# Kernel tuning notes

Hardware: AMD Instinct MI355X
Metric: run time of the kernel (lower is better)

The kernel has to match this reference:

```python
import jax, jax.numpy as jnp
import numpy as np

HEADS = 16
HEAD_DIM = 128


def rotate_half(x):
    x1, x2 = jnp.split(x, 2, axis=-1)
    return jnp.concatenate((-x2, x1), axis=-1)


def setup_inputs() -> dict:
    key = jax.random.key(0)
    ks = jax.random.split(key, 8)
    b, s, h = 2, 2048, 2048
    x = jax.random.normal(ks[0], (b, s, h), dtype=jnp.float32)
    attention_mask = jnp.zeros((1, 1, s, s), dtype=jnp.float32)
    alibi = jax.random.normal(ks[1], (1, HEADS, 1, s), dtype=jnp.float32)
    freqs = jax.random.normal(ks[2], (1, 1, s, HEAD_DIM), dtype=jnp.float32)
    scale = 1.0 / np.sqrt(h)
    Wq = jax.random.normal(ks[3], (h, h), dtype=jnp.float32) * scale
    Wk = jax.random.normal(ks[4], (h, h), dtype=jnp.float32) * scale
    Wv = jax.random.normal(ks[5], (h, h), dtype=jnp.float32) * scale
    Wo = jax.random.normal(ks[6], (h, h), dtype=jnp.float32) * scale
    return {"x": x, "attention_mask": attention_mask, "alibi": alibi,
            "freqs": freqs, "Wq": Wq, "Wk": Wk, "Wv": Wv, "Wo": Wo}


def reference(x, attention_mask, alibi, freqs, Wq, Wk, Wv, Wo):
    b, s, hidden = x.shape
    # torch Linear: y = x @ W.T (weight shape [out, in])
    def proj(W):
        y = x @ W.T
        return y.reshape(b, s, HEADS, HEAD_DIM).transpose(0, 2, 1, 3)  # [b,H,s,d]
    q, k, v = proj(Wq), proj(Wk), proj(Wv)
    cos, sin = jnp.cos(freqs), jnp.sin(freqs)
    q = q * cos + rotate_half(q) * sin
    k = k * cos + rotate_half(k) * sin
    scores = jnp.einsum('bhqd,bhkd->bhqk', q, k) / np.sqrt(HEAD_DIM)
    scores = scores + attention_mask + alibi
    attn = jax.nn.softmax(scores, axis=-1)
    out = jnp.einsum('bhqk,bhkd->bhqd', attn, v)
    out = out.transpose(0, 2, 1, 3).reshape(b, s, hidden)
    return out @ Wo.T
```

## Files before the change

kernel.cpp:

```cpp
#include <hip/hip_runtime.h>
#include <math.h>

typedef __attribute__((ext_vector_type(8))) short short8;
typedef __attribute__((ext_vector_type(4))) float f32x4;
typedef __attribute__((ext_vector_type(4))) unsigned short us4;
typedef __attribute__((ext_vector_type(4))) float fl4;

#define B_ 2
#define S_ 2048
#define H_ 16
#define D_ 128
#define HID 2048

__device__ __forceinline__ unsigned short f2bf(float f){
  unsigned u = __builtin_bit_cast(unsigned, f);
  u += 0x7fffu + ((u >> 16) & 1u);
  return (unsigned short)(u >> 16);
}
__device__ __forceinline__ float bf2f(unsigned short u){
  unsigned x = ((unsigned)u) << 16;
  return __builtin_bit_cast(float, x);
}

__device__ __forceinline__ void g2lds16(const unsigned short* g, unsigned short* l){
  __builtin_amdgcn_global_load_lds(
      (const __attribute__((address_space(1))) unsigned int*)g,
      (__attribute__((address_space(3))) unsigned int*)l, 16, 0, 0);
}

__global__ void cvt_k(const float* __restrict__ src, unsigned short* __restrict__ dst){
  int i = (blockIdx.x * 256 + threadIdx.x) * 4;
  fl4 v = *(const fl4*)(src + i);
  us4 o;
  #pragma unroll
  for (int t = 0; t < 4; t++) o[t] = f2bf(v[t]);
  *(us4*)(dst + i) = o;
}

__global__ void tab_k(const float* __restrict__ freqs, float* __restrict__ ctab,
                      float* __restrict__ stab){
  int i = blockIdx.x * 256 + threadIdx.x;
  float f = freqs[i];
  ctab[i] = cosf(f);
  stab[i] = sinf(f);
}

template<int EPI>
__global__ __launch_bounds__(256) void gemm_k(
    const unsigned short* __restrict__ A,
    const unsigned short* __restrict__ B0,
    const unsigned short* __restrict__ B1,
    unsigned short* __restrict__ O0,
    unsigned short* __restrict__ O1,
    float* __restrict__ Of)
{
  __shared__ __align__(16) unsigned short As[128 * 32];
  __shared__ __align__(16) unsigned short Bs[128 * 32];
  const int tid = threadIdx.x;
  const int l = tid & 63, lg = l >> 4, lr = l & 15;
  const int w = tid >> 6, wm = w & 1, wn = w >> 1;
  const int m0 = blockIdx.x * 128, n0 = blockIdx.y * 128;
  const unsigned short* Bm = (EPI == 1 && blockIdx.z == 1) ? B1 : B0;

  f32x4 acc[4][4];
  #pragma unroll
  for (int i = 0; i < 4; i++)
    #pragma unroll
    for (int j = 0; j < 4; j++)
      acc[i][j] = f32x4{0.f, 0.f, 0.f, 0.f};

  const unsigned short* gA = A  + (size_t)(m0 + (tid >> 2)) * HID + (tid & 3) * 8;
  const unsigned short* gB = Bm + (size_t)(n0 + (tid >> 2)) * HID + (tid & 3) * 8;
  unsigned short* lA = As + tid * 8;
  unsigned short* lB = Bs + tid * 8;

  for (int kt = 0; kt < HID; kt += 32){
    __syncthreads();
    g2lds16(gA + kt,            lA);
    g2lds16(gA + 64 * HID + kt, lA + 2048);
    g2lds16(gB + kt,            lB);
    g2lds16(gB + 64 * HID + kt, lB + 2048);
    __syncthreads();

    short8 aF[4], bF[4];
    #pragma unroll
    for (int mi = 0; mi < 4; mi++)
      aF[mi] = *(const short8*)(As + (wm * 64 + mi * 16 + lr) * 32 + lg * 8);
    #pragma unroll
    for (int ni = 0; ni < 4; ni++)
      bF[ni] = *(const short8*)(Bs + (wn * 64 + ni * 16 + lr) * 32 + lg * 8);
    #pragma unroll
    for (int mi = 0; mi < 4; mi++)
      #pragma unroll
      for (int ni = 0; ni < 4; ni++)
        acc[mi][ni] = __builtin_amdgcn_mfma_f32_16x16x32_bf16(aF[mi], bF[ni], acc[mi][ni], 0, 0, 0);
  }

  if (EPI == 1){
    unsigned short* O = blockIdx.z ? O1 : O0;
    #pragma unroll
    for (int mi = 0; mi < 4; mi++)
      #pragma unroll
      for (int r = 0; r < 4; r++){
        int i = m0 + wm * 64 + mi * 16 + lg * 4 + r;
        int b = i >> 11, s = i & 2047;
        #pragma unroll
        for (int ni = 0; ni < 4; ni++){
          int j = n0 + wn * 64 + ni * 16 + lr;
          int h = j >> 7, d = j & 127;
          O[((size_t)(b * H_ + h) * S_ + s) * D_ + d] = f2bf(acc[mi][ni][r]);
        }
      }
  } else if (EPI == 2){
    #pragma unroll
    for (int mi = 0; mi < 4; mi++)
      #pragma unroll
      for (int r = 0; r < 4; r++){
        int gi = m0 + wm * 64 + mi * 16 + lg * 4 + r;
        int h = gi >> 7, d = gi & 127;
        #pragma unroll
        for (int ni = 0; ni < 4; ni++){
          int gj = n0 + wn * 64 + ni * 16 + lr;
          int b = gj >> 11, s = gj & 2047;
          O0[((size_t)(b * H_ + h) * D_ + d) * S_ + s] = f2bf(acc[mi][ni][r]);
        }
      }
  } else {
    #pragma unroll
    for (int mi = 0; mi < 4; mi++)
      #pragma unroll
      for (int r = 0; r < 4; r++){
        int i = m0 + wm * 64 + mi * 16 + lg * 4 + r;
        #pragma unroll
        for (int ni = 0; ni < 4; ni++){
          int j = n0 + wn * 64 + ni * 16 + lr;
          Of[(size_t)i * HID + j] = acc[mi][ni][r];
        }
      }
  }
}

__global__ void rope_k(unsigned short* __restrict__ Q, unsigned short* __restrict__ K,
                       const float* __restrict__ ctab, const float* __restrict__ stab){
  int idx = blockIdx.x * 256 + threadIdx.x;
  unsigned short* P = (idx >= (1 << 20)) ? K : Q;
  int e  = idx & ((1 << 20) - 1);
  int g  = e & 15;
  int s  = (e >> 4) & 2047;
  int bh = e >> 15;
  int d0 = g * 4;
  size_t base = ((size_t)bh * S_ + s) * D_;
  us4 qa = *(us4*)(P + base + d0);
  us4 qb = *(us4*)(P + base + d0 + 64);
  fl4 ca = *(const fl4*)(ctab + s * D_ + d0);
  fl4 sa = *(const fl4*)(stab + s * D_ + d0);
  fl4 cb = *(const fl4*)(ctab + s * D_ + d0 + 64);
  fl4 sb = *(const fl4*)(stab + s * D_ + d0 + 64);
  us4 oa, ob;
  #pragma unroll
  for (int t = 0; t < 4; t++){
    float xa = bf2f(qa[t]), xb = bf2f(qb[t]);
    oa[t] = f2bf(xa * ca[t] - xb * sa[t]);
    ob[t] = f2bf(xb * cb[t] + xa * sb[t]);
  }
  *(us4*)(P + base + d0)      = oa;
  *(us4*)(P + base + d0 + 64) = ob;
}

__global__ __launch_bounds__(256) void attn_k(
    const unsigned short* __restrict__ Q,
    const unsigned short* __restrict__ Kg,
    const unsigned short* __restrict__ Vt,
    const float* __restrict__ mask,
    const float* __restrict__ alibi,
    unsigned short* __restrict__ Ctx)
{
  __shared__ __align__(16) unsigned short Kl[64 * 128];
  __shared__ __align__(16) unsigned short Vl[128 * 64];
  const int tid = threadIdx.x;
  const int l = tid & 63, lg = l >> 4, lr = l & 15;
  const int w = tid >> 6;
  const int bh = blockIdx.y, b = bh >> 4, h = bh & 15;
  const int q0 = blockIdx.x * 64 + w * 16;
  const size_t hb = (size_t)bh * S_ * D_;
  const float* mrow = mask + (size_t)(q0 + lr) * S_;
  const float* al = alibi + h * S_;
  const int sidx = (l & 48) + ((l & 48) >> 2);
  const float SCL2E = 0.08838834764831845f * 1.4426950408889634f;
  const float L2E = 1.4426950408889634f;

  const int krow = tid >> 2;
  const int vrow = tid >> 1;
  const unsigned short* gK = Kg + hb + (size_t)krow * D_ + (tid & 3) * 32;
  const unsigned short* gV = Vt + hb + (size_t)vrow * S_ + (tid & 1) * 32;
  int kw[4], vw[4];
  #pragma unroll
  for (int i = 0; i < 4; i++){
    kw[i] = krow * 128 + ((((tid & 3) * 4 + i) ^ (krow & 7)) * 8);
    vw[i] = vrow * 64  + ((((tid & 1) * 4 + i) ^ (vrow & 7)) * 8);
  }

  short8 qf[4];
  #pragma unroll
  for (int c = 0; c < 4; c++)
    qf[c] = *(const short8*)(Q + hb + (size_t)(q0 + lr) * D_ + c * 32 + lg * 8);

  f32x4 acc[8];
  #pragma unroll
  for (int c = 0; c < 8; c++) acc[c] = f32x4{0.f, 0.f, 0.f, 0.f};
  float mr = -1e30f, lsum = 0.f;

  for (int t = 0; t < 32; t++){
    const int kv0 = t * 64;
    short8 ks[4], vs[4];
    #pragma unroll
    for (int i = 0; i < 4; i++) ks[i] = *(const short8*)(gK + (size_t)kv0 * D_ + i * 8);
    #pragma unroll
    for (int i = 0; i < 4; i++) vs[i] = *(const short8*)(gV + kv0 + i * 8);
    __syncthreads();
    #pragma unroll
    for (int i = 0; i < 4; i++) *(short8*)(Kl + kw[i]) = ks[i];
    #pragma unroll
    for (int i = 0; i < 4; i++) *(short8*)(Vl + vw[i]) = vs[i];
    __syncthreads();

    f32x4 sg[4];
    #pragma unroll
    for (int g = 0; g < 4; g++) sg[g] = f32x4{0.f, 0.f, 0.f, 0.f};
    #pragma unroll
    for (int g = 0; g < 4; g++){
      const int row = g * 16 + lr;
      #pragma unroll
      for (int c = 0; c < 4; c++){
        short8 kf = *(const short8*)(Kl + row * 128 + (((c * 4 + lg) ^ (row & 7)) * 8));
        sg[g] = __builtin_amdgcn_mfma_f32_16x16x32_bf16(kf, qf[c], sg[g], 0, 0, 0);
      }
    }

    float x[4][4];
    #pragma unroll
    for (int g = 0; g < 4; g++){
      fl4 mk = *(const fl4*)(mrow + kv0 + g * 16 + 4 * lg);
      fl4 aa = *(const fl4*)(al  + kv0 + g * 16 + 4 * lg);
      #pragma unroll
      for (int r = 0; r < 4; r++)
        x[g][r] = fmaf(sg[g][r], SCL2E, (mk[r] + aa[r]) * L2E);
    }
    float mx = -1e30f;
    #pragma unroll
    for (int g = 0; g < 4; g++)
      #pragma unroll
      for (int r = 0; r < 4; r++) mx = fmaxf(mx, x[g][r]);
    mx = fmaxf(mx, __shfl_xor(mx, 16));
    mx = fmaxf(mx, __shfl_xor(mx, 32));
    float mnew = fmaxf(mr, mx);
    float alpha = exp2f(mr - mnew);
    float p[4][4], ps = 0.f;
    #pragma unroll
    for (int g = 0; g < 4; g++)
      #pragma unroll
      for (int r = 0; r < 4; r++){
        p[g][r] = exp2f(x[g][r] - mnew);
        ps += p[g][r];
      }
    ps += __shfl_xor(ps, 16);
    ps += __shfl_xor(ps, 32);
    lsum = lsum * alpha + ps;
    mr = mnew;

    int pk0[4], pk1[4];
    #pragma unroll
    for (int r = 0; r < 4; r++){
      pk0[r] = ((int)(unsigned)f2bf(p[1][r]) << 16) | (int)(unsigned)f2bf(p[0][r]);
      pk1[r] = ((int)(unsigned)f2bf(p[3][r]) << 16) | (int)(unsigned)f2bf(p[2][r]);
    }

    float ar[4];
    #pragma unroll
    for (int r = 0; r < 4; r++) ar[r] = __shfl(alpha, sidx + r);
    #pragma unroll
    for (int c = 0; c < 8; c++)
      #pragma unroll
      for (int r = 0; r < 4; r++) acc[c][r] *= ar[r];

    const int srcb = lr + ((lg & 1) << 5);
    short8 af0, af1;
    #pragma unroll
    for (int j = 0; j < 8; j++){
      int w0 = __shfl(pk0[j & 3], srcb + ((j >> 2) << 4));
      int w1 = __shfl(pk1[j & 3], srcb + ((j >> 2) << 4));
      af0[j] = (short)((l & 32) ? ((unsigned)w0 >> 16) : ((unsigned)w0 & 0xffffu));
      af1[j] = (short)((l & 32) ? ((unsigned)w1 >> 16) : ((unsigned)w1 & 0xffffu));
    }

    #pragma unroll
    for (int c = 0; c < 8; c++){
      const int d0 = c * 16 + lr;
      short8 vf0 = *(const short8*)(Vl + d0 * 64 + ((lg       ^ (d0 & 7)) * 8));
      short8 vf1 = *(const short8*)(Vl + d0 * 64 + (((4 + lg) ^ (d0 & 7)) * 8));
      acc[c] = __builtin_amdgcn_mfma_f32_16x16x32_bf16(af0, vf0, acc[c], 0, 0, 0);
      acc[c] = __builtin_amdgcn_mfma_f32_16x16x32_bf16(af1, vf1, acc[c], 0, 0, 0);
    }
  }

  float inv = 1.f / lsum;
  float ir[4];
  #pragma unroll
  for (int r = 0; r < 4; r++) ir[r] = __shfl(inv, sidx + r);
  #pragma unroll
  for (int r = 0; r < 4; r++){
    const int qg = q0 + 4 * lg + r;
    const size_t ob = ((size_t)(b * S_ + qg) * H_ + h) * D_;
    #pragma unroll
    for (int c = 0; c < 8; c++)
      Ctx[ob + c * 16 + lr] = f2bf(acc[c][r] * ir[r]);
  }
}

extern "C" void kernel_launch(void* const* d_in, const int* in_sizes, int n_in,
                              void* d_out, int out_size, void* d_ws, size_t ws_size,
                              hipStream_t stream){
  const float* x     = (const float*)d_in[0];
  const float* mask  = (const float*)d_in[1];
  const float* alibi = (const float*)d_in[2];
  const float* freqs = (const float*)d_in[3];
  const float* Wq    = (const float*)d_in[4];
  const float* Wk    = (const float*)d_in[5];
  const float* Wv    = (const float*)d_in[6];
  const float* Wo    = (const float*)d_in[7];
  float* out = (float*)d_out;

  unsigned short* ws  = (unsigned short*)d_ws;
  unsigned short* xb  = ws;
  unsigned short* wqb = ws + 8388608;
  unsigned short* wkb = ws + 12582912;
  unsigned short* wvb = ws + 16777216;
  unsigned short* wob = ws + 20971520;
  unsigned short* Qb  = ws + 25165824;
  unsigned short* Kb  = ws + 33554432;
  unsigned short* Vb  = ws + 41943040;
  unsigned short* ctx = xb;
  float* ctab = (float*)(ws + 50331648);
  float* stab = ctab + 262144;

  cvt_k<<<8192, 256, 0, stream>>>(x,  xb);
  cvt_k<<<4096, 256, 0, stream>>>(Wq, wqb);
  cvt_k<<<4096, 256, 0, stream>>>(Wk, wkb);
  cvt_k<<<4096, 256, 0, stream>>>(Wv, wvb);
  cvt_k<<<4096, 256, 0, stream>>>(Wo, wob);
  tab_k<<<1024, 256, 0, stream>>>(freqs, ctab, stab);

  gemm_k<1><<<dim3(32, 16, 2), 256, 0, stream>>>(xb, wqb, wkb, Qb, Kb, nullptr);
  gemm_k<2><<<dim3(16, 32, 1), 256, 0, stream>>>(wvb, xb, nullptr, Vb, nullptr, nullptr);
  rope_k<<<8192, 256, 0, stream>>>(Qb, Kb, ctab, stab);
  attn_k<<<dim3(32, 32), 256, 0, stream>>>(Qb, Kb, Vb, mask, alibi, ctx);
  gemm_k<0><<<dim3(32, 16, 1), 256, 0, stream>>>(ctx, wob, nullptr, nullptr, nullptr, out);
}
```

Measured before the change: 573.1 us.

## Double-buffer GEMM and attention tiles with async LDS loads, lazy softmax rescale

Both the GEMM and the attention kernel now use two LDS buffers. Each kernel issues global_load_lds for the next tile before computing on the current one, which drops one barrier per iteration and overlaps loads with MFMA work. In attention, K and V go directly to swizzled LDS through direct loads instead of a register round-trip, and the mask and alibi loads are hoisted ahead of the QK matmul. The online softmax also skips the max and rescale step when the tile max stays within a threshold of the running max, and packs bf16 with v_cvt_pk_bf16_f32. The cost is twice the LDS per block, which may reduce occupancy, and a small change in numeric behaviour from the deferred max.

```diff
diff --git a/kernel.cpp b/kernel.cpp
--- a/kernel.cpp
+++ b/kernel.cpp
@@ -20,6 +20,9 @@
 __device__ __forceinline__ float bf2f(unsigned short u){
   unsigned x = ((unsigned)u) << 16;
   return __builtin_bit_cast(float, x);
+}
+__device__ __forceinline__ int cvtpk(float lo, float hi){
+  int r; asm("v_cvt_pk_bf16_f32 %0, %1, %2" : "=v"(r) : "v"(lo), "v"(hi)); return r;
 }
 
 __device__ __forceinline__ void g2lds16(const unsigned short* g, unsigned short* l){
@@ -54,8 +57,8 @@
     unsigned short* __restrict__ O1,
     float* __restrict__ Of)
 {
-  __shared__ __align__(16) unsigned short As[128 * 32];
-  __shared__ __align__(16) unsigned short Bs[128 * 32];
+  __shared__ __align__(16) unsigned short As[2][128 * 32];
+  __shared__ __align__(16) unsigned short Bs[2][128 * 32];
   const int tid = threadIdx.x;
   const int l = tid & 63, lg = l >> 4, lr = l & 15;
   const int w = tid >> 6, wm = w & 1, wn = w >> 1;
@@ -71,30 +74,35 @@
 
   const unsigned short* gA = A  + (size_t)(m0 + (tid >> 2)) * HID + (tid & 3) * 8;
   const unsigned short* gB = Bm + (size_t)(n0 + (tid >> 2)) * HID + (tid & 3) * 8;
-  unsigned short* lA = As + tid * 8;
-  unsigned short* lB = Bs + tid * 8;
-
-  for (int kt = 0; kt < HID; kt += 32){
-    __syncthreads();
-    g2lds16(gA + kt,            lA);
-    g2lds16(gA + 64 * HID + kt, lA + 2048);
-    g2lds16(gB + kt,            lB);
-    g2lds16(gB + 64 * HID + kt, lB + 2048);
-    __syncthreads();
-
+
+  #define GSTAGE(buf, kt) do {                                   \
+    g2lds16(gA + (kt),            As[buf] + tid * 8);            \
+    g2lds16(gA + 64 * HID + (kt), As[buf] + 2048 + tid * 8);     \
+    g2lds16(gB + (kt),            Bs[buf] + tid * 8);            \
+    g2lds16(gB + 64 * HID + (kt), Bs[buf] + 2048 + tid * 8);     \
+  } while (0)
+
+  GSTAGE(0, 0);
+  __syncthreads();
+  int cur = 0;
+  for (int t = 0; t < 64; t++){
+    if (t < 63) GSTAGE(cur ^ 1, (t + 1) * 32);
     short8 aF[4], bF[4];
     #pragma unroll
     for (int mi = 0; mi < 4; mi++)
-      aF[mi] = *(const short8*)(As + (wm * 64 + mi * 16 + lr) * 32 + lg * 8);
+      aF[mi] = *(const short8*)(As[cur] + (wm * 64 + mi * 16 + lr) * 32 + lg * 8);
     #pragma unroll
     for (int ni = 0; ni < 4; ni++)
-      bF[ni] = *(const short8*)(Bs + (wn * 64 + ni * 16 + lr) * 32 + lg * 8);
+      bF[ni] = *(const short8*)(Bs[cur] + (wn * 64 + ni * 16 + lr) * 32 + lg * 8);
     #pragma unroll
     for (int mi = 0; mi < 4; mi++)
       #pragma unroll
       for (int ni = 0; ni < 4; ni++)
         acc[mi][ni] = __builtin_amdgcn_mfma_f32_16x16x32_bf16(aF[mi], bF[ni], acc[mi][ni], 0, 0, 0);
-  }
+    __syncthreads();
+    cur ^= 1;
+  }
+  #undef GSTAGE
 
   if (EPI == 1){
     unsigned short* O = blockIdx.z ? O1 : O0;
@@ -175,8 +183,8 @@
     const float* __restrict__ alibi,
     unsigned short* __restrict__ Ctx)
 {
-  __shared__ __align__(16) unsigned short Kl[64 * 128];
-  __shared__ __align__(16) unsigned short Vl[128 * 64];
+  __shared__ __align__(16) unsigned short Kl[2][64 * 128];
+  __shared__ __align__(16) unsigned short Vl[2][128 * 64];
   const int tid = threadIdx.x;
   const int l = tid & 63, lg = l >> 4, lr = l & 15;
   const int w = tid >> 6;
@@ -189,16 +197,26 @@
   const float SCL2E = 0.08838834764831845f * 1.4426950408889634f;
   const float L2E = 1.4426950408889634f;
 
-  const int krow = tid >> 2;
-  const int vrow = tid >> 1;
-  const unsigned short* gK = Kg + hb + (size_t)krow * D_ + (tid & 3) * 32;
-  const unsigned short* gV = Vt + hb + (size_t)vrow * S_ + (tid & 1) * 32;
-  int kw[4], vw[4];
-  #pragma unroll
-  for (int i = 0; i < 4; i++){
-    kw[i] = krow * 128 + ((((tid & 3) * 4 + i) ^ (krow & 7)) * 8);
-    vw[i] = vrow * 64  + ((((tid & 1) * 4 + i) ^ (vrow & 7)) * 8);
-  }
+  const int kswz = (((tid & 15) ^ ((tid >> 4) & 7)) * 8);
+  const unsigned short* gK = Kg + hb + (size_t)(tid >> 4) * D_ + kswz;
+  const int vswz = (((tid & 7) ^ ((tid >> 3) & 7)) * 8);
+  const unsigned short* gV = Vt + hb + (size_t)(tid >> 3) * S_ + vswz;
+
+  #define ASTAGE(buf, kv)  do {                                            \
+    g2lds16(gK + (size_t)((kv))      * D_, Kl[buf] + tid * 8);             \
+    g2lds16(gK + (size_t)((kv) + 16) * D_, Kl[buf] + 2048 + tid * 8);      \
+    g2lds16(gK + (size_t)((kv) + 32) * D_, Kl[buf] + 4096 + tid * 8);      \
+    g2lds16(gK + (size_t)((kv) + 48) * D_, Kl[buf] + 6144 + tid * 8);      \
+    g2lds16(gV + (kv),                     Vl[buf] + tid * 8);             \
+    g2lds16(gV + 32 * S_ + (kv),           Vl[buf] + 2048 + tid * 8);      \
+    g2lds16(gV + 64 * S_ + (kv),           Vl[buf] + 4096 + tid * 8);      \
+    g2lds16(gV + 96 * S_ + (kv),           Vl[buf] + 6144 + tid * 8);      \
+  } while (0)
+
+  int koff[4];
+  #pragma unroll
+  for (int c = 0; c < 4; c++) koff[c] = ((c * 4 + lg) ^ (lr & 7)) * 8;
+  const int vo0 = (lg ^ (lr & 7)) * 8, vo1 = ((4 + lg) ^ (lr & 7)) * 8;
 
   short8 qf[4];
   #pragma unroll
@@ -210,19 +228,20 @@
   for (int c = 0; c < 8; c++) acc[c] = f32x4{0.f, 0.f, 0.f, 0.f};
   float mr = -1e30f, lsum = 0.f;
 
+  ASTAGE(0, 0);
+  __syncthreads();
+  int cur = 0;
+
   for (int t = 0; t < 32; t++){
     const int kv0 = t * 64;
-    short8 ks[4], vs[4];
-    #pragma unroll
-    for (int i = 0; i < 4; i++) ks[i] = *(const short8*)(gK + (size_t)kv0 * D_ + i * 8);
-    #pragma unroll
-    for (int i = 0; i < 4; i++) vs[i] = *(const short8*)(gV + kv0 + i * 8);
-    __syncthreads();
-    #pragma unroll
-    for (int i = 0; i < 4; i++) *(short8*)(Kl + kw[i]) = ks[i];
-    #pragma unroll
-    for (int i = 0; i < 4; i++) *(short8*)(Vl + vw[i]) = vs[i];
-    __syncthreads();
+    if (t < 31) ASTAGE(cur ^ 1, kv0 + 64);
+
+    fl4 mk[4], aa[4];
+    #pragma unroll
+    for (int g = 0; g < 4; g++){
+      mk[g] = *(const fl4*)(mrow + kv0 + g * 16 + 4 * lg);
+      aa[g] = *(const fl4*)(al  + kv0 + g * 16 + 4 * lg);
+    }
 
     f32x4 sg[4];
     #pragma unroll
@@ -232,56 +251,67 @@
       const int row = g * 16 + lr;
       #pragma unroll
       for (int c = 0; c < 4; c++){
-        short8 kf = *(const short8*)(Kl + row * 128 + (((c * 4 + lg) ^ (row & 7)) * 8));
+        short8 kf = *(const short8*)(Kl[cur] + row * 128 + koff[c]);
         sg[g] = __builtin_amdgcn_mfma_f32_16x16x32_bf16(kf, qf[c], sg[g], 0, 0, 0);
       }
     }
 
     float x[4][4];
     #pragma unroll
-    for (int g = 0; g < 4; g++){
-      fl4 mk = *(const fl4*)(mrow + kv0 + g * 16 + 4 * lg);
-      fl4 aa = *(const fl4*)(al  + kv0 + g * 16 + 4 * lg);
+    for (int g = 0; g < 4; g++)
       #pragma unroll
       for (int r = 0; r < 4; r++)
-        x[g][r] = fmaf(sg[g][r], SCL2E, (mk[r] + aa[r]) * L2E);
-    }
+        x[g][r] = fmaf(sg[g][r], SCL2E, (mk[g][r] + aa[g][r]) * L2E);
+
     float mx = -1e30f;
     #pragma unroll
     for (int g = 0; g < 4; g++)
       #pragma unroll
       for (int r = 0; r < 4; r++) mx = fmaxf(mx, x[g][r]);
-    mx = fmaxf(mx, __shfl_xor(mx, 16));
-    mx = fmaxf(mx, __shfl_xor(mx, 32));
-    float mnew = fmaxf(mr, mx);
-    float alpha = exp2f(mr - mnew);
+
     float p[4][4], ps = 0.f;
-    #pragma unroll
-    for (int g = 0; g < 4; g++)
-      #pragma unroll
-      for (int r = 0; r < 4; r++){
-        p[g][r] = exp2f(x[g][r] - mnew);
-        ps += p[g][r];
-      }
-    ps += __shfl_xor(ps, 16);
-    ps += __shfl_xor(ps, 32);
-    lsum = lsum * alpha + ps;
-    mr = mnew;
+    if (__all(mx <= mr + 8.f)){
+      #pragma unroll
+      for (int g = 0; g < 4; g++)
+        #pragma unroll
+        for (int r = 0; r < 4; r++){
+          p[g][r] = exp2f(x[g][r] - mr);
+          ps += p[g][r];
+        }
+      ps += __shfl_xor(ps, 16);
+      ps += __shfl_xor(ps, 32);
+      lsum += ps;
+    } else {
+      mx = fmaxf(mx, __shfl_xor(mx, 16));
+      mx = fmaxf(mx, __shfl_xor(mx, 32));
+      float mnew = fmaxf(mr, mx);
+      float alpha = exp2f(mr - mnew);
+      #pragma unroll
+      for (int g = 0; g < 4; g++)
+        #pragma unroll
+        for (int r = 0; r < 4; r++){
+          p[g][r] = exp2f(x[g][r] - mnew);
+          ps += p[g][r];
+        }
+      ps += __shfl_xor(ps, 16);
+      ps += __shfl_xor(ps, 32);
+      lsum = lsum * alpha + ps;
+      mr = mnew;
+      float ar[4];
+      #pragma unroll
+      for (int r = 0; r < 4; r++) ar[r] = __shfl(alpha, sidx + r);
+      #pragma unroll
+      for (int c = 0; c < 8; c++)
+        #pragma unroll
+        for (int r = 0; r < 4; r++) acc[c][r] *= ar[r];
+    }
 
     int pk0[4], pk1[4];
     #pragma unroll
     for (int r = 0; r < 4; r++){
-      pk0[r] = ((int)(unsigned)f2bf(p[1][r]) << 16) | (int)(unsigned)f2bf(p[0][r]);
-      pk1[r] = ((int)(unsigned)f2bf(p[3][r]) << 16) | (int)(unsigned)f2bf(p[2][r]);
-    }
-
-    float ar[4];
-    #pragma unroll
-    for (int r = 0; r < 4; r++) ar[r] = __shfl(alpha, sidx + r);
-    #pragma unroll
-    for (int c = 0; c < 8; c++)
-      #pragma unroll
-      for (int r = 0; r < 4; r++) acc[c][r] *= ar[r];
+      pk0[r] = cvtpk(p[0][r], p[1][r]);
+      pk1[r] = cvtpk(p[2][r], p[3][r]);
+    }
 
     const int srcb = lr + ((lg & 1) << 5);
     short8 af0, af1;
@@ -296,12 +326,16 @@
     #pragma unroll
     for (int c = 0; c < 8; c++){
       const int d0 = c * 16 + lr;
-      short8 vf0 = *(const short8*)(Vl + d0 * 64 + ((lg       ^ (d0 & 7)) * 8));
-      short8 vf1 = *(const short8*)(Vl + d0 * 64 + (((4 + lg) ^ (d0 & 7)) * 8));
+      short8 vf0 = *(const short8*)(Vl[cur] + d0 * 64 + vo0);
+      short8 vf1 = *(const short8*)(Vl[cur] + d0 * 64 + vo1);
       acc[c] = __builtin_amdgcn_mfma_f32_16x16x32_bf16(af0, vf0, acc[c], 0, 0, 0);
       acc[c] = __builtin_amdgcn_mfma_f32_16x16x32_bf16(af1, vf1, acc[c], 0, 0, 0);
     }
-  }
+
+    __syncthreads();
+    cur ^= 1;
+  }
+  #undef ASTAGE
 
   float inv = 1.f / lsum;
   float ir[4];
```

Measured after the change: 562.3 us. Within noise of the previous version (-1.9%).
